# Kernel tuning notes

Measured on AMD Instinct MI355X. Metric: run time of the kernel, lower is better.

## Reference

```python
import jax, jax.numpy as jnp
import numpy as np

DECAY = 0.99
EPS = 1e-05


def setup_inputs() -> dict:
    key = jax.random.key(0)
    k1, k2, k3 = jax.random.split(key, 3)
    x = jax.random.normal(k1, (16, 4096, 512), dtype=jnp.float32)
    embed = jax.random.normal(k2, (1024, 512), dtype=jnp.float32)
    cluster_size = jnp.ones((1024,), dtype=jnp.float32)
    embed_avg = jax.random.normal(k3, (1024, 512), dtype=jnp.float32)
    return {"x": x, "embed": embed, "cluster_size": cluster_size, "embed_avg": embed_avg}


def reference(x, embed, cluster_size, embed_avg):
    # x: [..., d]; embed: [K, d]
    K, d = embed.shape
    xf = x.reshape(-1, d)  # [N, d]
    dist = -(jnp.sum(xf * xf, axis=1, keepdims=True)
             - 2.0 * (xf @ embed.T)
             + jnp.sum(embed * embed, axis=1)[None, :])  # [N, K]
    ind = jnp.argmax(dist, axis=-1)  # [N]
    quantize = embed[ind].reshape(x.shape)  # dequantize (embedding lookup)
    embed_ind = ind.reshape(x.shape[:-1])
    # Training-mode EMA updates (one-hot scatter expressed as segment adds)
    counts = jnp.zeros((K,), dtype=x.dtype).at[ind].add(1.0)           # onehot.sum(0)
    embed_sum = jnp.zeros((K, d), dtype=x.dtype).at[ind].add(xf)       # (x^T @ onehot)^T
    new_cluster_size = cluster_size * DECAY + (1.0 - DECAY) * counts
    new_embed_avg = embed_avg * DECAY + (1.0 - DECAY) * embed_sum
    n = jnp.sum(new_cluster_size)
    cs = (new_cluster_size + EPS) / (n + K * EPS) * n  # laplace smoothing * total
    new_embed = new_embed_avg / cs[:, None]
    return (quantize, embed_ind, new_cluster_size, new_embed_avg, new_embed)
```

## Files before the change

### kernel.cpp

```cpp
#include <hip/hip_runtime.h>

typedef unsigned short ushort_t;
typedef __attribute__((ext_vector_type(8))) short bf16x8;
typedef __attribute__((ext_vector_type(4))) float f32x4;

#define DECAY 0.99f
#define EPS 1e-5f
#define K_CODES 1024
#define D 512
#define N_ROWS 65536
#define MARGIN 0.0625f

#define BM 128
#define NKT 8
#define NCH 16

#define CHUNK 64
#define MAX_CHUNKS 2048

#define XH_OFF   0u
#define XL_OFF   67108864u
#define EH_OFF   134217728u
#define EL_OFF   135266304u
#define ESUM_OFF 136314880u
#define CNT_OFF  138412032u
#define E2_OFF   138416128u
#define NFLAG_OFF 138420224u
#define NPTR_OFF  138420228u
#define FLAGS_OFF 138420480u
#define WS_NEED  (138420480u + 262144u)
#define ROWLIST_OFF   0u
#define BASE_OFF      262144u
#define CURSOR_OFF    266240u
#define CHUNKBASE_OFF 270336u
#define DESC_OFF      274432u
#define PARTIAL_OFF   307200u

__device__ inline ushort_t f2bf(float f) {
    unsigned int u = __float_as_uint(f);
    unsigned int r = (u + 0x7FFFu + ((u >> 16) & 1u)) >> 16;
    return (ushort_t)r;
}
__device__ inline float bf2f(ushort_t h) { return __uint_as_float(((unsigned int)h) << 16); }

__device__ inline void gload16_lds(const void* g, void* l) {
    __builtin_amdgcn_global_load_lds(
        (const __attribute__((address_space(1))) unsigned int*)g,
        (__attribute__((address_space(3))) unsigned int*)l, 16, 0, 0);
}

__global__ __launch_bounds__(256) void prep_split(const float* __restrict__ src,
                                                  ushort_t* __restrict__ hi,
                                                  ushort_t* __restrict__ lo) {
    const int g = blockIdx.x * 256 + threadIdx.x;
    const int ln = g & 63;
    const int tc = g >> 6;
    const int C = tc & 15;
    const int R = tc >> 4;
    const int row = (R << 4) + (ln & 15);
    const int k = (C << 5) + ((ln >> 4) << 3);
    const float4 v0 = *(const float4*)(src + (size_t)row * D + k);
    const float4 v1 = *(const float4*)(src + (size_t)row * D + k + 4);
    float v[8] = {v0.x, v0.y, v0.z, v0.w, v1.x, v1.y, v1.z, v1.w};
    short h[8], l[8];
    #pragma unroll
    for (int i = 0; i < 8; ++i) {
        ushort_t hh = f2bf(v[i]);
        h[i] = (short)hh;
        l[i] = (short)f2bf(v[i] - bf2f(hh));
    }
    bf16x8 hv = {h[0], h[1], h[2], h[3], h[4], h[5], h[6], h[7]};
    bf16x8 lv = {l[0], l[1], l[2], l[3], l[4], l[5], l[6], l[7]};
    *(bf16x8*)(hi + (size_t)g * 8) = hv;
    *(bf16x8*)(lo + (size_t)g * 8) = lv;
}

__global__ __launch_bounds__(64) void e2_kernel(const float* __restrict__ embed,
                                                float* __restrict__ e2) {
    const int k = blockIdx.x;
    const int t = threadIdx.x;
    const float* row = embed + (size_t)k * D;
    float s = 0.f;
    #pragma unroll
    for (int i = 0; i < D / 64; ++i) {
        float v = row[t + 64 * i];
        s = fmaf(v, v, s);
    }
    #pragma unroll
    for (int off = 32; off; off >>= 1) s += __shfl_down(s, off, 64);
    if (t == 0) e2[k] = s;
}

__global__ __launch_bounds__(256, 2) void vq_main(const ushort_t* __restrict__ xh,
                                                  const ushort_t* __restrict__ xl,
                                                  const ushort_t* __restrict__ eh,
                                                  const ushort_t* __restrict__ el,
                                                  const float* __restrict__ embed,
                                                  const float* __restrict__ e2,
                                                  float* __restrict__ out_q,
                                                  float* __restrict__ out_ind,
                                                  float* __restrict__ counts,
                                                  int* __restrict__ nflag,
                                                  int* __restrict__ flags) {
    __shared__ short sAh[2][4096], sAl[2][4096], sBh[2][4096], sBl[2][4096];
    __shared__ float se2[1024];
    __shared__ float red_b[128][2], red_s[128][2];
    __shared__ int   red_i[128][2];
    __shared__ int   bestk[128];

    const int tid = threadIdx.x;
    const int lane = tid & 63;
    const int w = tid >> 6;
    const int wm = w & 1;
    const int wn = w >> 1;
    const int bid = ((int)blockIdx.x & 7) * 64 + ((int)blockIdx.x >> 3);
    const int R0 = bid * 8;
    const int row0 = bid * BM;

    for (int i = tid; i < 1024; i += 256) se2[i] = e2[i];

    const int ltile = lane << 3;

    #define STAGE(nk, nc, B) do {                                                              \
        if (w == 0) {                                                                          \
            _Pragma("unroll")                                                                  \
            for (int t = 0; t < 8; ++t)                                                        \
                gload16_lds(xh + ((size_t)((R0 + t) * 16 + (nc)) << 9) + ltile,                \
                            &sAh[(B)][t << 9]);                                                \
        } else if (w == 1) {                                                                   \
            _Pragma("unroll")                                                                  \
            for (int t = 0; t < 8; ++t)                                                        \
                gload16_lds(xl + ((size_t)((R0 + t) * 16 + (nc)) << 9) + ltile,                \
                            &sAl[(B)][t << 9]);                                                \
        } else if (w == 2) {                                                                   \
            _Pragma("unroll")                                                                  \
            for (int t = 0; t < 8; ++t)                                                        \
                gload16_lds(eh + ((size_t)((((nk) << 3) + t) * 16 + (nc)) << 9) + ltile,       \
                            &sBh[(B)][t << 9]);                                                \
        } else {                                                                               \
            _Pragma("unroll")                                                                  \
            for (int t = 0; t < 8; ++t)                                                        \
                gload16_lds(el + ((size_t)((((nk) << 3) + t) * 16 + (nc)) << 9) + ltile,       \
                            &sBl[(B)][t << 9]);                                                \
        }                                                                                      \
    } while (0)

    float tb[16], ts[16];
    int ti[16];
    #pragma unroll
    for (int s = 0; s < 16; ++s) { tb[s] = -3.4e38f; ts[s] = -3.4e38f; ti[s] = 0; }

    STAGE(0, 0, 0);
    __syncthreads();
    int cur = 0;

    for (int kt = 0; kt < NKT; ++kt) {
        f32x4 acc[4][4];
        #pragma unroll
        for (int mt = 0; mt < 4; ++mt)
            #pragma unroll
            for (int nt = 0; nt < 4; ++nt) acc[mt][nt] = (f32x4){0.f, 0.f, 0.f, 0.f};

        for (int c = 0; c < NCH; ++c) {
            const int nxt = cur ^ 1;
            if (!(kt == NKT - 1 && c == NCH - 1)) {
                const int nk = (c == NCH - 1) ? kt + 1 : kt;
                const int nc = (c == NCH - 1) ? 0 : c + 1;
                STAGE(nk, nc, nxt);
            }

            bf16x8 ah[4], al4[4], bh[4], bl[4];
            #pragma unroll
            for (int i = 0; i < 4; ++i) {
                ah[i]  = *(const bf16x8*)(&sAh[cur][(((wm << 2) + i) << 9) + ltile]);
                al4[i] = *(const bf16x8*)(&sAl[cur][(((wm << 2) + i) << 9) + ltile]);
                bh[i]  = *(const bf16x8*)(&sBh[cur][(((wn << 2) + i) << 9) + ltile]);
                bl[i]  = *(const bf16x8*)(&sBl[cur][(((wn << 2) + i) << 9) + ltile]);
            }
            #pragma unroll
            for (int nt = 0; nt < 4; ++nt) {
                #pragma unroll
                for (int mt = 0; mt < 4; ++mt) {
                    acc[mt][nt] = __builtin_amdgcn_mfma_f32_16x16x32_bf16(ah[mt], bh[nt], acc[mt][nt], 0, 0, 0);
                    acc[mt][nt] = __builtin_amdgcn_mfma_f32_16x16x32_bf16(al4[mt], bh[nt], acc[mt][nt], 0, 0, 0);
                    acc[mt][nt] = __builtin_amdgcn_mfma_f32_16x16x32_bf16(ah[mt], bl[nt], acc[mt][nt], 0, 0, 0);
                }
            }
            __syncthreads();
            cur = nxt;
        }

        #pragma unroll
        for (int nt = 0; nt < 4; ++nt) {
            const int code = (kt << 7) + (wn << 6) + (nt << 4) + (lane & 15);
            const float h = se2[code];
            #pragma unroll
            for (int mt = 0; mt < 4; ++mt) {
                #pragma unroll
                for (int r = 0; r < 4; ++r) {
                    const float v = fmaf(-0.5f, h, acc[mt][nt][r]);
                    const int s = (mt << 2) + r;
                    if (v > tb[s]) { ts[s] = tb[s]; tb[s] = v; ti[s] = code; }
                    else if (v > ts[s]) ts[s] = v;
                }
            }
        }
    }
    #undef STAGE

    #pragma unroll
    for (int m = 1; m <= 8; m <<= 1) {
        #pragma unroll
        for (int s = 0; s < 16; ++s) {
            const float ob = __shfl_xor(tb[s], m, 64);
            const float os = __shfl_xor(ts[s], m, 64);
            const int oi = __shfl_xor(ti[s], m, 64);
            if (ob > tb[s] || (ob == tb[s] && oi < ti[s])) {
                ts[s] = fmaxf(tb[s], os); tb[s] = ob; ti[s] = oi;
            } else {
                ts[s] = fmaxf(ts[s], ob);
            }
        }
    }
    if ((lane & 15) == 0) {
        const int q = lane >> 4;
        #pragma unroll
        for (int mt = 0; mt < 4; ++mt)
            #pragma unroll
            for (int r = 0; r < 4; ++r) {
                const int rl = wm * 64 + mt * 16 + q * 4 + r;
                const int s = (mt << 2) + r;
                red_b[rl][wn] = tb[s]; red_s[rl][wn] = ts[s]; red_i[rl][wn] = ti[s];
            }
    }
    __syncthreads();

    if (tid < BM) {
        float b0 = red_b[tid][0], b1 = red_b[tid][1];
        float s0 = red_s[tid][0], s1 = red_s[tid][1];
        int i0 = red_i[tid][0], i1 = red_i[tid][1];
        float b, sec; int bi;
        if (b0 > b1 || (b0 == b1 && i0 < i1)) { b = b0; bi = i0; sec = fmaxf(s0, b1); }
        else { b = b1; bi = i1; sec = fmaxf(s1, b0); }
        bestk[tid] = bi;
        out_ind[row0 + tid] = (float)bi;
        atomicAdd(counts + bi, 1.0f);
        if (b - sec < MARGIN) {
            const int p = atomicAdd(nflag, 1);
            flags[p] = row0 + tid;
        }
    }
    __syncthreads();

    {
        const int f4 = tid & 127;
        const int rodd = tid >> 7;
        for (int it = 0; it < 64; ++it) {
            const int r = 2 * it + rodd;
            const int bk = bestk[r];
            const float4 q = ((const float4*)(embed + (size_t)bk * D))[f4];
            ((float4*)(out_q + (size_t)(row0 + r) * D))[f4] = q;
        }
    }
}

__global__ __launch_bounds__(256) void fixup(const float* __restrict__ x,
                                             const float* __restrict__ embed,
                                             const float* __restrict__ e2,
                                             const int* __restrict__ nflag,
                                             const int* __restrict__ flags,
                                             float* __restrict__ out_ind,
                                             float* __restrict__ out_q,
                                             float* __restrict__ counts) {
    __shared__ float xs[D];
    __shared__ float rb[256];
    __shared__ int ri[256];
    __shared__ int s_new;
    const int tid = threadIdx.x;
    const int n = *nflag;
    for (int fi = blockIdx.x; fi < n; fi += gridDim.x) {
        const int row = flags[fi];
        if (tid < 128) ((float4*)xs)[tid] = ((const float4*)(x + (size_t)row * D))[tid];
        __syncthreads();
        float best = -3.4e38f; int bi = 0;
        #pragma unroll
        for (int j = 0; j < 4; ++j) {
            const int c = tid * 4 + j;
            float acc = 0.f;
            const float4* ep = (const float4*)(embed + (size_t)c * D);
            for (int i4 = 0; i4 < 128; ++i4) {
                const float4 ev = ep[i4];
                const float4 xv = ((const float4*)xs)[i4];
                acc = fmaf(ev.x, xv.x, acc);
                acc = fmaf(ev.y, xv.y, acc);
                acc = fmaf(ev.z, xv.z, acc);
                acc = fmaf(ev.w, xv.w, acc);
            }
            const float sc = fmaf(-0.5f, e2[c], acc);
            if (sc > best) { best = sc; bi = c; }
        }
        rb[tid] = best; ri[tid] = bi;
        __syncthreads();
        for (int off = 128; off; off >>= 1) {
            if (tid < off) {
                if (rb[tid + off] > rb[tid] ||
                    (rb[tid + off] == rb[tid] && ri[tid + off] < ri[tid])) {
                    rb[tid] = rb[tid + off]; ri[tid] = ri[tid + off];
                }
            }
            __syncthreads();
        }
        if (tid == 0) {
            const int newi = ri[0];
            const int oldi = (int)out_ind[row];
            s_new = (newi == oldi) ? -1 : newi;
            if (newi != oldi) {
                out_ind[row] = (float)newi;
                atomicAdd(counts + oldi, -1.0f);
                atomicAdd(counts + newi, 1.0f);
            }
        }
        __syncthreads();
        const int nw = s_new;
        if (nw >= 0 && tid < 128) {
            const float4 q = ((const float4*)(embed + (size_t)nw * D))[tid];
            ((float4*)(out_q + (size_t)row * D))[tid] = q;
        }
        __syncthreads();
    }
}

__global__ __launch_bounds__(1024) void scan_kernel(const float* __restrict__ counts,
                                                    int* __restrict__ base,
                                                    int* __restrict__ cursor,
                                                    int* __restrict__ chunk_base,
                                                    int4* __restrict__ desc) {
    __shared__ int s[1024];
    const int t = threadIdx.x;
    const int c = (int)counts[t];
    s[t] = c;
    __syncthreads();
    #pragma unroll
    for (int off = 1; off < 1024; off <<= 1) {
        const int v = (t >= off) ? s[t - off] : 0;
        __syncthreads();
        s[t] += v;
        __syncthreads();
    }
    const int b = s[t] - c;
    base[t] = b;
    cursor[t] = b;
    const int nch = (c + CHUNK - 1) / CHUNK;
    s[t] = nch;
    __syncthreads();
    #pragma unroll
    for (int off = 1; off < 1024; off <<= 1) {
        const int v = (t >= off) ? s[t - off] : 0;
        __syncthreads();
        s[t] += v;
        __syncthreads();
    }
    const int cb = s[t] - nch;
    chunk_base[t] = cb;
    if (t == 1023) chunk_base[1024] = s[t];
    for (int j = 0; j < nch; ++j) {
        const int start = b + j * CHUNK;
        const int len = min(CHUNK, c - j * CHUNK);
        desc[cb + j] = make_int4(t, start, len, 0);
    }
}

__global__ __launch_bounds__(256) void scatter_kernel(const float* __restrict__ out_ind,
                                                      int* __restrict__ cursor,
                                                      int* __restrict__ rowlist) {
    const int g = blockIdx.x * 256 + threadIdx.x;
    const int code = (int)out_ind[g];
    const int pos = atomicAdd(cursor + code, 1);
    rowlist[pos] = g;
}

__global__ __launch_bounds__(128) void esum_partial(const float* __restrict__ x,
                                                    const int* __restrict__ chunk_base,
                                                    const int4* __restrict__ desc,
                                                    const int* __restrict__ rowlist,
                                                    float* __restrict__ partial) {
    const int b = blockIdx.x;
    if (b >= chunk_base[1024]) return;
    const int t = threadIdx.x;
    const int4 d = desc[b];
    const int b0 = d.y;
    const int cnt = d.z;
    float4 a0 = {0.f, 0.f, 0.f, 0.f}, a1 = {0.f, 0.f, 0.f, 0.f};
    float4 a2 = {0.f, 0.f, 0.f, 0.f}, a3 = {0.f, 0.f, 0.f, 0.f};
    int i = 0;
    for (; i + 4 <= cnt; i += 4) {
        const int r0 = rowlist[b0 + i];
        const int r1 = rowlist[b0 + i + 1];
        const int r2 = rowlist[b0 + i + 2];
        const int r3 = rowlist[b0 + i + 3];
        const float4 v0 = ((const float4*)x)[(size_t)r0 * 128 + t];
        const float4 v1 = ((const float4*)x)[(size_t)r1 * 128 + t];
        const float4 v2 = ((const float4*)x)[(size_t)r2 * 128 + t];
        const float4 v3 = ((const float4*)x)[(size_t)r3 * 128 + t];
        a0.x += v0.x; a0.y += v0.y; a0.z += v0.z; a0.w += v0.w;
        a1.x += v1.x; a1.y += v1.y; a1.z += v1.z; a1.w += v1.w;
        a2.x += v2.x; a2.y += v2.y; a2.z += v2.z; a2.w += v2.w;
        a3.x += v3.x; a3.y += v3.y; a3.z += v3.z; a3.w += v3.w;
    }
    for (; i < cnt; ++i) {
        const int r = rowlist[b0 + i];
        const float4 v = ((const float4*)x)[(size_t)r * 128 + t];
        a0.x += v.x; a0.y += v.y; a0.z += v.z; a0.w += v.w;
    }
    float4 s;
    s.x = (a0.x + a1.x) + (a2.x + a3.x);
    s.y = (a0.y + a1.y) + (a2.y + a3.y);
    s.z = (a0.z + a1.z) + (a2.z + a3.z);
    s.w = (a0.w + a1.w) + (a2.w + a3.w);
    ((float4*)partial)[(size_t)b * 128 + t] = s;
}

__global__ __launch_bounds__(128) void esum_final(const int* __restrict__ chunk_base,
                                                  const float* __restrict__ partial,
                                                  float* __restrict__ embed_sum) {
    const int k = blockIdx.x;
    const int t = threadIdx.x;
    const int c0 = chunk_base[k];
    const int c1 = chunk_base[k + 1];
    float4 a = {0.f, 0.f, 0.f, 0.f};
    for (int c = c0; c < c1; ++c) {
        const float4 v = ((const float4*)partial)[(size_t)c * 128 + t];
        a.x += v.x; a.y += v.y; a.z += v.z; a.w += v.w;
    }
    ((float4*)embed_sum)[(size_t)k * 128 + t] = a;
}

__global__ __launch_bounds__(256) void ema_cs(const float* __restrict__ cs,
                                              const float* __restrict__ counts,
                                              float* __restrict__ out_cs,
                                              float* __restrict__ nout) {
    __shared__ float red[256];
    const int t = threadIdx.x;
    const float4 c4 = ((const float4*)counts)[t];
    const float4 s4 = ((const float4*)cs)[t];
    float4 nc;
    nc.x = s4.x * DECAY + (1.f - DECAY) * c4.x;
    nc.y = s4.y * DECAY + (1.f - DECAY) * c4.y;
    nc.z = s4.z * DECAY + (1.f - DECAY) * c4.z;
    nc.w = s4.w * DECAY + (1.f - DECAY) * c4.w;
    ((float4*)out_cs)[t] = nc;
    red[t] = nc.x + nc.y + nc.z + nc.w;
    __syncthreads();
    #pragma unroll
    for (int off = 128; off; off >>= 1) {
        if (t < off) red[t] += red[t + off];
        __syncthreads();
    }
    if (t == 0) nout[0] = red[0];
}

__global__ __launch_bounds__(256) void ema_embed(const float* __restrict__ eavg,
                                                 const float* __restrict__ esum,
                                                 const float* __restrict__ ncs,
                                                 const float* __restrict__ nptr,
                                                 float* __restrict__ out_avg,
                                                 float* __restrict__ out_embed) {
    const int i4 = blockIdx.x * 256 + threadIdx.x;
    const int k = i4 >> 7;
    const float n = *nptr;
    const float csk = (ncs[k] + EPS) / (n + (float)K_CODES * EPS) * n;
    const float inv = 1.f / csk;
    const float4 a = ((const float4*)eavg)[i4];
    const float4 s = ((const float4*)esum)[i4];
    float4 na;
    na.x = a.x * DECAY + (1.f - DECAY) * s.x;
    na.y = a.y * DECAY + (1.f - DECAY) * s.y;
    na.z = a.z * DECAY + (1.f - DECAY) * s.z;
    na.w = a.w * DECAY + (1.f - DECAY) * s.w;
    ((float4*)out_avg)[i4] = na;
    float4 ne;
    ne.x = na.x * inv; ne.y = na.y * inv; ne.z = na.z * inv; ne.w = na.w * inv;
    ((float4*)out_embed)[i4] = ne;
}

#define MT2 128
#define S_STRIDE 132
__global__ __launch_bounds__(256, 2) void vq_main_f32(const float* __restrict__ x,
                                                      const float* __restrict__ embed,
                                                      const float* __restrict__ e2,
                                                      float* __restrict__ out_q,
                                                      float* __restrict__ out_ind,
                                                      float* __restrict__ counts,
                                                      float* __restrict__ embed_sum) {
    __shared__ float xs[32][S_STRIDE];
    __shared__ float es[32][S_STRIDE];
    __shared__ float rsc[MT2][17];
    __shared__ int rid[MT2][17];
    __shared__ int bestk[MT2];
    const int tid = threadIdx.x;
    const int lane = tid & 63;
    const int w = tid >> 6;
    const int tyg = (w & 1) * 8 + (lane >> 3);
    const int txg = (w >> 1) * 8 + (lane & 7);
    const int r0 = 8 * tyg, c0 = 8 * txg;
    const int row0 = blockIdx.x * MT2;
    const int sr = tid >> 3, sq = tid & 7;
    float best_s[8]; int best_i[8];
    #pragma unroll
    for (int r = 0; r < 8; ++r) { best_s[r] = -3.4e38f; best_i[r] = 0; }
    float4 px[4], pe[4];
    #pragma unroll
    for (int i = 0; i < 4; ++i) {
        px[i] = *(const float4*)(x + (size_t)(row0 + sr + 32 * i) * D + sq * 4);
        pe[i] = *(const float4*)(embed + (size_t)(sr + 32 * i) * D + sq * 4);
    }
    for (int kt = 0; kt < 8; ++kt) {
        const int k0 = kt * 128;
        float acc[8][8];
        #pragma unroll
        for (int j = 0; j < 8; ++j) {
            const float he = -0.5f * e2[k0 + c0 + j];
            #pragma unroll
            for (int r = 0; r < 8; ++r) acc[r][j] = he;
        }
        for (int dt = 0; dt < 16; ++dt) {
            __syncthreads();
            #pragma unroll
            for (int i = 0; i < 4; ++i) {
                const int rr = sr + 32 * i;
                #pragma unroll
                for (int ii = 0; ii < 4; ++ii) {
                    xs[sq * 4 + ii][rr] = ((const float*)&px[i])[ii];
                    es[sq * 4 + ii][rr] = ((const float*)&pe[i])[ii];
                }
            }
            __syncthreads();
            {
                const int s2 = kt * 16 + dt + 1;
                int kt2 = s2 >> 4; if (kt2 > 7) kt2 = 7;
                const int dt2 = s2 & 15;
                const int dof = dt2 * 32 + sq * 4;
                #pragma unroll
                for (int i = 0; i < 4; ++i) {
                    px[i] = *(const float4*)(x + (size_t)(row0 + sr + 32 * i) * D + dof);
                    pe[i] = *(const float4*)(embed + (size_t)(kt2 * 128 + sr + 32 * i) * D + dof);
                }
            }
            #pragma unroll 4
            for (int d = 0; d < 32; ++d) {
                const float4 xa = *(const float4*)&xs[d][r0];
                const float4 xb = *(const float4*)&xs[d][r0 + 4];
                const float4 ea = *(const float4*)&es[d][c0];
                const float4 eb = *(const float4*)&es[d][c0 + 4];
                const float xv[8] = {xa.x, xa.y, xa.z, xa.w, xb.x, xb.y, xb.z, xb.w};
                const float evv[8] = {ea.x, ea.y, ea.z, ea.w, eb.x, eb.y, eb.z, eb.w};
                #pragma unroll
                for (int r = 0; r < 8; ++r)
                    #pragma unroll
                    for (int j = 0; j < 8; ++j)
                        acc[r][j] = fmaf(xv[r], evv[j], acc[r][j]);
            }
        }
        #pragma unroll
        for (int j = 0; j < 8; ++j) {
            const int k = k0 + c0 + j;
            #pragma unroll
            for (int r = 0; r < 8; ++r)
                if (acc[r][j] > best_s[r]) { best_s[r] = acc[r][j]; best_i[r] = k; }
        }
    }
    #pragma unroll
    for (int r = 0; r < 8; ++r) { rsc[r0 + r][txg] = best_s[r]; rid[r0 + r][txg] = best_i[r]; }
    __syncthreads();
    if (tid < MT2) {
        float bs = rsc[tid][0]; int bk = rid[tid][0];
        #pragma unroll
        for (int g = 1; g < 16; ++g) {
            const float s = rsc[tid][g]; const int kk = rid[tid][g];
            if (s > bs || (s == bs && kk < bk)) { bs = s; bk = kk; }
        }
        bestk[tid] = bk;
        out_ind[row0 + tid] = (float)bk;
        atomicAdd(counts + bk, 1.0f);
    }
    __syncthreads();
    {
        const int f4 = tid & 127, rodd = tid >> 7;
        for (int it = 0; it < 64; ++it) {
            const int r = 2 * it + rodd;
            const int bk = bestk[r];
            const float4 q = ((const float4*)(embed + (size_t)bk * D))[f4];
            ((float4*)(out_q + (size_t)(row0 + r) * D))[f4] = q;
            const float4 xv = ((const float4*)(x + (size_t)(row0 + r) * D))[f4];
            float* sdst = embed_sum + (size_t)bk * D + f4 * 4;
            atomicAdd(sdst + 0, xv.x);
            atomicAdd(sdst + 1, xv.y);
            atomicAdd(sdst + 2, xv.z);
            atomicAdd(sdst + 3, xv.w);
        }
    }
}

extern "C" void kernel_launch(void* const* d_in, const int* in_sizes, int n_in,
                              void* d_out, int out_size, void* d_ws, size_t ws_size,
                              hipStream_t stream) {
    const float* x     = (const float*)d_in[0];
    const float* embed = (const float*)d_in[1];
    const float* cs    = (const float*)d_in[2];
    const float* eavg  = (const float*)d_in[3];

    float* out = (float*)d_out;
    float* out_q   = out;
    float* out_ind = out_q + (size_t)N_ROWS * D;
    float* out_cs  = out_ind + N_ROWS;
    float* out_avg = out_cs + K_CODES;
    float* out_emb = out_avg + (size_t)K_CODES * D;

    unsigned char* w = (unsigned char*)d_ws;

    if (ws_size >= WS_NEED) {
        ushort_t* xh = (ushort_t*)(w + XH_OFF);
        ushort_t* xl = (ushort_t*)(w + XL_OFF);
        ushort_t* eh = (ushort_t*)(w + EH_OFF);
        ushort_t* el = (ushort_t*)(w + EL_OFF);
        float* esum  = (float*)(w + ESUM_OFF);
        float* counts = (float*)(w + CNT_OFF);
        float* e2    = (float*)(w + E2_OFF);
        int* nflag   = (int*)(w + NFLAG_OFF);
        float* nptr  = (float*)(w + NPTR_OFF);
        int* flags   = (int*)(w + FLAGS_OFF);
        int* rowlist    = (int*)(w + ROWLIST_OFF);
        int* base       = (int*)(w + BASE_OFF);
        int* cursor     = (int*)(w + CURSOR_OFF);
        int* chunk_base = (int*)(w + CHUNKBASE_OFF);
        int4* desc      = (int4*)(w + DESC_OFF);
        float* partial  = (float*)(w + PARTIAL_OFF);

        hipMemsetAsync(counts, 0, 4096, stream);
        hipMemsetAsync(nflag, 0, 4, stream);
        prep_split<<<16384, 256, 0, stream>>>(x, xh, xl);
        prep_split<<<256, 256, 0, stream>>>(embed, eh, el);
        e2_kernel<<<K_CODES, 64, 0, stream>>>(embed, e2);
        vq_main<<<N_ROWS / BM, 256, 0, stream>>>(xh, xl, eh, el, embed, e2,
                                                 out_q, out_ind, counts, nflag, flags);
        fixup<<<1024, 256, 0, stream>>>(x, embed, e2, nflag, flags,
                                        out_ind, out_q, counts);
        scan_kernel<<<1, 1024, 0, stream>>>(counts, base, cursor, chunk_base, desc);
        scatter_kernel<<<N_ROWS / 256, 256, 0, stream>>>(out_ind, cursor, rowlist);
        esum_partial<<<MAX_CHUNKS, 128, 0, stream>>>(x, chunk_base, desc, rowlist, partial);
        esum_final<<<K_CODES, 128, 0, stream>>>(chunk_base, partial, esum);
        ema_cs<<<1, 256, 0, stream>>>(cs, counts, out_cs, nptr);
        ema_embed<<<(K_CODES * D / 4) / 256, 256, 0, stream>>>(eavg, esum, out_cs, nptr,
                                                               out_avg, out_emb);
    } else {
        float* counts = (float*)w;
        float* esum = counts + K_CODES;
        float* e2 = esum + (size_t)K_CODES * D;
        float* nptr = e2 + K_CODES;
        hipMemsetAsync(counts, 0, (size_t)(K_CODES + K_CODES * D) * sizeof(float), stream);
        e2_kernel<<<K_CODES, 64, 0, stream>>>(embed, e2);
        vq_main_f32<<<N_ROWS / MT2, 256, 0, stream>>>(x, embed, e2, out_q, out_ind, counts, esum);
        ema_cs<<<1, 256, 0, stream>>>(cs, counts, out_cs, nptr);
        ema_embed<<<(K_CODES * D / 4) / 256, 256, 0, stream>>>(eavg, esum, out_cs, nptr,
                                                               out_avg, out_emb);
    }
}
```

Before: 755.9 us.

## Drop bf16 hi/lo split and use single bf16 matmul with wider fixup margin

The split-bf16 (hi+lo, three MFMAs) distance GEMM is replaced by a single bf16 MFMA per tile, removing the lo-part prep writes, LDS buffers and two-thirds of the matrix math. To compensate for the lower precision, the top-2 margin that flags rows for exact fp32 re-check in the fixup kernel grows from 0.0625 to 1.0. Launch bounds are raised to 3 blocks per CU since LDS use halves. The risk is that many more rows get flagged, which makes the fixup pass more expensive, and correctness depends on the margin covering the bf16 error.

```diff
diff --git a/kernel.cpp b/kernel.cpp
--- a/kernel.cpp
+++ b/kernel.cpp
@@ -9,7 +9,7 @@
 #define K_CODES 1024
 #define D 512
 #define N_ROWS 65536
-#define MARGIN 0.0625f
+#define MARGIN 1.0f
 
 #define BM 128
 #define NKT 8
@@ -49,9 +49,8 @@
         (__attribute__((address_space(3))) unsigned int*)l, 16, 0, 0);
 }
 
-__global__ __launch_bounds__(256) void prep_split(const float* __restrict__ src,
-                                                  ushort_t* __restrict__ hi,
-                                                  ushort_t* __restrict__ lo) {
+__global__ __launch_bounds__(256) void prep_hi(const float* __restrict__ src,
+                                               ushort_t* __restrict__ hi) {
     const int g = blockIdx.x * 256 + threadIdx.x;
     const int ln = g & 63;
     const int tc = g >> 6;
@@ -62,17 +61,11 @@
     const float4 v0 = *(const float4*)(src + (size_t)row * D + k);
     const float4 v1 = *(const float4*)(src + (size_t)row * D + k + 4);
     float v[8] = {v0.x, v0.y, v0.z, v0.w, v1.x, v1.y, v1.z, v1.w};
-    short h[8], l[8];
-    #pragma unroll
-    for (int i = 0; i < 8; ++i) {
-        ushort_t hh = f2bf(v[i]);
-        h[i] = (short)hh;
-        l[i] = (short)f2bf(v[i] - bf2f(hh));
-    }
+    short h[8];
+    #pragma unroll
+    for (int i = 0; i < 8; ++i) h[i] = (short)f2bf(v[i]);
     bf16x8 hv = {h[0], h[1], h[2], h[3], h[4], h[5], h[6], h[7]};
-    bf16x8 lv = {l[0], l[1], l[2], l[3], l[4], l[5], l[6], l[7]};
     *(bf16x8*)(hi + (size_t)g * 8) = hv;
-    *(bf16x8*)(lo + (size_t)g * 8) = lv;
 }
 
 __global__ __launch_bounds__(64) void e2_kernel(const float* __restrict__ embed,
@@ -91,10 +84,8 @@
     if (t == 0) e2[k] = s;
 }
 
-__global__ __launch_bounds__(256, 2) void vq_main(const ushort_t* __restrict__ xh,
-                                                  const ushort_t* __restrict__ xl,
+__global__ __launch_bounds__(256, 3) void vq_main(const ushort_t* __restrict__ xh,
                                                   const ushort_t* __restrict__ eh,
-                                                  const ushort_t* __restrict__ el,
                                                   const float* __restrict__ embed,
                                                   const float* __restrict__ e2,
                                                   float* __restrict__ out_q,
@@ -102,7 +93,7 @@
                                                   float* __restrict__ counts,
                                                   int* __restrict__ nflag,
                                                   int* __restrict__ flags) {
-    __shared__ short sAh[2][4096], sAl[2][4096], sBh[2][4096], sBl[2][4096];
+    __shared__ short sAh[2][4096], sBh[2][4096];
     __shared__ float se2[1024];
     __shared__ float red_b[128][2], red_s[128][2];
     __shared__ int   red_i[128][2];
@@ -120,28 +111,19 @@
     for (int i = tid; i < 1024; i += 256) se2[i] = e2[i];
 
     const int ltile = lane << 3;
+    const int whalf = (w & 1) << 2;
 
     #define STAGE(nk, nc, B) do {                                                              \
-        if (w == 0) {                                                                          \
+        if (w < 2) {                                                                           \
             _Pragma("unroll")                                                                  \
-            for (int t = 0; t < 8; ++t)                                                        \
-                gload16_lds(xh + ((size_t)((R0 + t) * 16 + (nc)) << 9) + ltile,                \
-                            &sAh[(B)][t << 9]);                                                \
-        } else if (w == 1) {                                                                   \
-            _Pragma("unroll")                                                                  \
-            for (int t = 0; t < 8; ++t)                                                        \
-                gload16_lds(xl + ((size_t)((R0 + t) * 16 + (nc)) << 9) + ltile,                \
-                            &sAl[(B)][t << 9]);                                                \
-        } else if (w == 2) {                                                                   \
-            _Pragma("unroll")                                                                  \
-            for (int t = 0; t < 8; ++t)                                                        \
-                gload16_lds(eh + ((size_t)((((nk) << 3) + t) * 16 + (nc)) << 9) + ltile,       \
-                            &sBh[(B)][t << 9]);                                                \
+            for (int t = 0; t < 4; ++t)                                                        \
+                gload16_lds(xh + ((size_t)((R0 + whalf + t) * 16 + (nc)) << 9) + ltile,        \
+                            &sAh[(B)][(whalf + t) << 9]);                                      \
         } else {                                                                               \
             _Pragma("unroll")                                                                  \
-            for (int t = 0; t < 8; ++t)                                                        \
-                gload16_lds(el + ((size_t)((((nk) << 3) + t) * 16 + (nc)) << 9) + ltile,       \
-                            &sBl[(B)][t << 9]);                                                \
+            for (int t = 0; t < 4; ++t)                                                        \
+                gload16_lds(eh + ((size_t)((((nk) << 3) + whalf + t) * 16 + (nc)) << 9) + ltile,\
+                            &sBh[(B)][(whalf + t) << 9]);                                      \
         }                                                                                      \
     } while (0)
 
@@ -169,21 +151,17 @@
                 STAGE(nk, nc, nxt);
             }
 
-            bf16x8 ah[4], al4[4], bh[4], bl[4];
+            bf16x8 ah[4], bh[4];
             #pragma unroll
             for (int i = 0; i < 4; ++i) {
-                ah[i]  = *(const bf16x8*)(&sAh[cur][(((wm << 2) + i) << 9) + ltile]);
-                al4[i] = *(const bf16x8*)(&sAl[cur][(((wm << 2) + i) << 9) + ltile]);
-                bh[i]  = *(const bf16x8*)(&sBh[cur][(((wn << 2) + i) << 9) + ltile]);
-                bl[i]  = *(const bf16x8*)(&sBl[cur][(((wn << 2) + i) << 9) + ltile]);
+                ah[i] = *(const bf16x8*)(&sAh[cur][(((wm << 2) + i) << 9) + ltile]);
+                bh[i] = *(const bf16x8*)(&sBh[cur][(((wn << 2) + i) << 9) + ltile]);
             }
             #pragma unroll
             for (int nt = 0; nt < 4; ++nt) {
                 #pragma unroll
                 for (int mt = 0; mt < 4; ++mt) {
                     acc[mt][nt] = __builtin_amdgcn_mfma_f32_16x16x32_bf16(ah[mt], bh[nt], acc[mt][nt], 0, 0, 0);
-                    acc[mt][nt] = __builtin_amdgcn_mfma_f32_16x16x32_bf16(al4[mt], bh[nt], acc[mt][nt], 0, 0, 0);
-                    acc[mt][nt] = __builtin_amdgcn_mfma_f32_16x16x32_bf16(ah[mt], bl[nt], acc[mt][nt], 0, 0, 0);
                 }
             }
             __syncthreads();
@@ -620,9 +598,7 @@
 
     if (ws_size >= WS_NEED) {
         ushort_t* xh = (ushort_t*)(w + XH_OFF);
-        ushort_t* xl = (ushort_t*)(w + XL_OFF);
         ushort_t* eh = (ushort_t*)(w + EH_OFF);
-        ushort_t* el = (ushort_t*)(w + EL_OFF);
         float* esum  = (float*)(w + ESUM_OFF);
         float* counts = (float*)(w + CNT_OFF);
         float* e2    = (float*)(w + E2_OFF);
@@ -638,10 +614,10 @@
 
         hipMemsetAsync(counts, 0, 4096, stream);
         hipMemsetAsync(nflag, 0, 4, stream);
-        prep_split<<<16384, 256, 0, stream>>>(x, xh, xl);
-        prep_split<<<256, 256, 0, stream>>>(embed, eh, el);
+        prep_hi<<<16384, 256, 0, stream>>>(x, xh);
+        prep_hi<<<256, 256, 0, stream>>>(embed, eh);
         e2_kernel<<<K_CODES, 64, 0, stream>>>(embed, e2);
-        vq_main<<<N_ROWS / BM, 256, 0, stream>>>(xh, xl, eh, el, embed, e2,
+        vq_main<<<N_ROWS / BM, 256, 0, stream>>>(xh, eh, embed, e2,
                                                  out_q, out_ind, counts, nflag, flags);
         fixup<<<1024, 256, 0, stream>>>(x, embed, e2, nflag, flags,
                                         out_ind, out_q, counts);
```

After: 2.437 ms. +222.4%, slower.
